# Optimization experiments

Hardware: AMD Instinct MI355X
Metric: run time of the kernel (lower is better)

## Reference

```python
import jax, jax.numpy as jnp
import numpy as np

HIDDEN = 768
NUM_HEADS = 12
HEAD_DIM = HIDDEN // NUM_HEADS
BIAS_SCALE = 0.5


def setup_inputs() -> dict:
    key = jax.random.key(0)
    ks = jax.random.split(key, 8)
    B, S = 4, 2048
    s = 1.0 / np.sqrt(HIDDEN)
    return {
        "hidden_states": jax.random.normal(ks[0], (B, S, HIDDEN), dtype=jnp.float32),
        "attention_mask": jnp.ones((B, S), dtype=jnp.float32),
        "Wq": jax.random.normal(ks[1], (HIDDEN, HIDDEN), dtype=jnp.float32) * s,
        "bq": jnp.zeros((HIDDEN,), dtype=jnp.float32),
        "Wk": jax.random.normal(ks[2], (HIDDEN, HIDDEN), dtype=jnp.float32) * s,
        "bk": jnp.zeros((HIDDEN,), dtype=jnp.float32),
        "Wv": jax.random.normal(ks[3], (HIDDEN, HIDDEN), dtype=jnp.float32) * s,
        "bv": jnp.zeros((HIDDEN,), dtype=jnp.float32),
        "head_bias": jnp.full((NUM_HEADS, 1, 1), 0.1, dtype=jnp.float32),
    }


def _split_heads(x):
    # [B,S,H] -> [B,nh,S,hd]
    B, S, _ = x.shape
    return x.reshape(B, S, NUM_HEADS, HEAD_DIM).transpose(0, 2, 1, 3)


def reference(hidden_states, attention_mask, Wq, bq, Wk, bk, Wv, bv, head_bias):
    q = _split_heads(hidden_states @ Wq.T + bq)
    k = _split_heads(hidden_states @ Wk.T + bk)
    v = _split_heads(hidden_states @ Wv.T + bv)
    # [B,nh,S,S]
    scores = jnp.einsum("bhqd,bhkd->bhqk", q, k) / np.sqrt(HEAD_DIM).astype(np.float32)
    scores = scores + BIAS_SCALE * head_bias  # head_bias broadcasts [nh,1,1]
    ext_mask = (1.0 - attention_mask[:, None, None, :]) * -10000.0
    scores = scores + ext_mask
    probs = jax.nn.softmax(scores, axis=-1)  # dropout is identity in eval
    ctx = jnp.einsum("bhqk,bhkd->bhqd", probs, v)
    B, _, S, _ = ctx.shape
    return ctx.transpose(0, 2, 1, 3).reshape(B, S, HIDDEN)
```

## Files before the change

kernel.cpp:

```cpp
#include <hip/hip_runtime.h>

#define LOG2E 1.44269504088896340736f
#define QSCALE 0.18033688011112042f
#define THR 8.0f

typedef _Float16 half8 __attribute__((ext_vector_type(8)));
typedef _Float16 half4_t __attribute__((ext_vector_type(4)));
typedef __fp16 fp16x2 __attribute__((ext_vector_type(2)));
typedef float f32x4 __attribute__((ext_vector_type(4)));
typedef float f32x16 __attribute__((ext_vector_type(16)));
typedef unsigned int u32x2 __attribute__((ext_vector_type(2)));

__device__ __forceinline__ void gld16(const void* g, void* l) {
  __builtin_amdgcn_global_load_lds(
      (const __attribute__((address_space(1))) void*)g,
      (__attribute__((address_space(3))) void*)l, 16, 0, 0);
}

__global__ void cvt_f32_f16(const float* __restrict__ src, _Float16* __restrict__ dst, int n4) {
  int i = blockIdx.x * blockDim.x + threadIdx.x;
  int st = gridDim.x * blockDim.x;
  for (; i < n4; i += st) {
    float4 v = reinterpret_cast<const float4*>(src)[i];
    half4_t h;
    h[0] = (_Float16)v.x; h[1] = (_Float16)v.y; h[2] = (_Float16)v.z; h[3] = (_Float16)v.w;
    reinterpret_cast<half4_t*>(dst)[i] = h;
  }
}

__global__ void prep_mask(const float* __restrict__ mask, float* __restrict__ mkb, int n) {
  int i = blockIdx.x * blockDim.x + threadIdx.x;
  if (i < n) mkb[i] = (1.0f - mask[i]) * (-10000.0f * LOG2E);
}

__global__ __launch_bounds__(256) void qkv_gemm(
    const _Float16* __restrict__ X,
    const _Float16* __restrict__ Wq, const _Float16* __restrict__ Wk, const _Float16* __restrict__ Wv,
    const float* __restrict__ bq, const float* __restrict__ bk, const float* __restrict__ bv,
    _Float16* __restrict__ qo, _Float16* __restrict__ ko, _Float16* __restrict__ vo) {
  __shared__ _Float16 Al[2][128 * 32];
  __shared__ _Float16 Bl[2][128 * 32];
  const int tid = threadIdx.x;
  const int lane = tid & 63, w = tid >> 6;
  const int wr = w >> 1, wc = w & 1;
  const int mt = blockIdx.x, ntl = blockIdx.y, mode = blockIdx.z;
  const _Float16* W = (mode == 0) ? Wq : (mode == 1) ? Wk : Wv;
  const float* bias = (mode == 0) ? bq : (mode == 1) ? bk : bv;
  _Float16* out = (mode == 0) ? qo : (mode == 1) ? ko : vo;
  const float oscale = (mode == 0) ? QSCALE : 1.0f;

  const _Float16* Xb = X + (size_t)mt * 128 * 768;
  const _Float16* Wb = W + (size_t)ntl * 128 * 768;

  const f32x4 zero4 = {0.f, 0.f, 0.f, 0.f};
  f32x4 acc[4][4];
#pragma unroll
  for (int i = 0; i < 4; ++i)
#pragma unroll
    for (int j = 0; j < 4; ++j) acc[i][j] = zero4;

  auto stage = [&](int bufi, int kt) {
#pragma unroll
    for (int it = 0; it < 2; ++it) {
      int ci = tid + it * 256;
      int row = ci >> 2, c = ci & 3;
      int sw = ((c ^ ((row >> 1) & 3)) << 4);
      gld16((const char*)(Xb + row * 768) + kt * 64 + sw, (char*)&Al[bufi][0] + ci * 16);
      gld16((const char*)(Wb + row * 768) + kt * 64 + sw, (char*)&Bl[bufi][0] + ci * 16);
    }
  };

  stage(0, 0);
  __syncthreads();
  int buf = 0;
  for (int kt = 0; kt < 24; ++kt) {
    if (kt + 1 < 24) stage(buf ^ 1, kt + 1);
    half8 af[4], bf[4];
#pragma unroll
    for (int mi = 0; mi < 4; ++mi) {
      int row = wr * 64 + mi * 16 + (lane & 15);
      int cc = (lane >> 4) ^ ((row >> 1) & 3);
      af[mi] = *(const half8*)((const char*)&Al[buf][0] + row * 64 + cc * 16);
    }
#pragma unroll
    for (int ni = 0; ni < 4; ++ni) {
      int row = wc * 64 + ni * 16 + (lane & 15);
      int cc = (lane >> 4) ^ ((row >> 1) & 3);
      bf[ni] = *(const half8*)((const char*)&Bl[buf][0] + row * 64 + cc * 16);
    }
#pragma unroll
    for (int mi = 0; mi < 4; ++mi)
#pragma unroll
      for (int ni = 0; ni < 4; ++ni)
        acc[mi][ni] = __builtin_amdgcn_mfma_f32_16x16x32_f16(af[mi], bf[ni], acc[mi][ni], 0, 0, 0);
    __syncthreads();
    buf ^= 1;
  }

  const int m0 = mt * 128 + wr * 64, n0 = ntl * 128 + wc * 64;
#pragma unroll
  for (int ni = 0; ni < 4; ++ni) {
    int n = n0 + ni * 16 + (lane & 15);
    float bvv = bias[n];
    int h = n >> 6, d = n & 63;
#pragma unroll
    for (int mi = 0; mi < 4; ++mi) {
      int m = m0 + mi * 16 + ((lane >> 4) << 2);
      int b = m >> 11, s = m & 2047;
      if (mode < 2) {
        _Float16* dst = out + (((size_t)(b * 12 + h) * 2048 + s) * 64 + d);
#pragma unroll
        for (int r = 0; r < 4; ++r) dst[(size_t)r * 64] = (_Float16)((acc[mi][ni][r] + bvv) * oscale);
      } else {
        half4_t pk;
#pragma unroll
        for (int r = 0; r < 4; ++r) pk[r] = (_Float16)(acc[mi][ni][r] + bvv);
        *(half4_t*)(out + ((size_t)(b * 12 + h) * 64 + d) * 2048 + s) = pk;
      }
    }
  }
}

__global__ __launch_bounds__(256) void flash_attn(
    const _Float16* __restrict__ qb, const _Float16* __restrict__ kbuf,
    const _Float16* __restrict__ vtb, const float* __restrict__ mkb,
    float* __restrict__ out) {
  __shared__ _Float16 Kl[2][64 * 64];
  __shared__ _Float16 Vl[2][64 * 64];
  __shared__ float Ml[2048];

  const int tid = threadIdx.x;
  const int lane = tid & 63, w = tid >> 6;
  const int l31 = lane & 31, hi32 = lane >> 5;

  const int i = blockIdx.x;
  const int bh = (i & 7) + 8 * ((i >> 3) >> 4);
  const int qt = (i >> 3) & 15;
  const int b = bh / 12, h = bh % 12;
  const int q0w = qt * 128 + w * 32;

  const _Float16* Kg = kbuf + (size_t)bh * 2048 * 64;
  const _Float16* Vg = vtb + (size_t)bh * 64 * 2048;

  half8 qf[4];
  {
    const _Float16* qp = qb + ((size_t)bh * 2048 + q0w + l31) * 64 + hi32 * 8;
#pragma unroll
    for (int c = 0; c < 4; ++c) qf[c] = *(const half8*)(qp + c * 16);
  }

  auto stage = [&](int nb, int t) {
#pragma unroll
    for (int it = 0; it < 2; ++it) {
      int ci = tid + it * 256;
      int row = ci >> 3, c = ci & 7;
      int sw = ((c ^ (row & 7)) << 4);
      gld16((const char*)Kg + (size_t)t * 8192 + row * 128 + sw, (char*)&Kl[nb][0] + ci * 16);
      gld16((const char*)Vg + (size_t)row * 4096 + t * 128 + sw, (char*)&Vl[nb][0] + ci * 16);
    }
  };

  {
    const char* ms = (const char*)(mkb + (size_t)b * 2048);
#pragma unroll
    for (int it = 0; it < 2; ++it) {
      int ci = tid + it * 256;
      gld16(ms + ci * 16, (char*)Ml + ci * 16);
    }
  }

  f32x16 o[2];
  float m_ = -3.0e4f, l_ = 0.f;
#pragma unroll
  for (int dt = 0; dt < 2; ++dt)
#pragma unroll
    for (int r = 0; r < 16; ++r) o[dt][r] = 0.f;

  stage(0, 0);
  __syncthreads();
  int buf = 0;

  for (int t = 0; t < 32; ++t) {
    if (t + 1 < 32) stage(buf ^ 1, t + 1);

    f32x4 mk[2][4];
    const float* mlt = Ml + t * 64 + hi32 * 4;
#pragma unroll
    for (int kt = 0; kt < 2; ++kt)
#pragma unroll
      for (int g = 0; g < 4; ++g) mk[kt][g] = *(const f32x4*)(mlt + kt * 32 + g * 8);

    const char* kb = (const char*)&Kl[buf][0];
    f32x16 sc[2];
    __builtin_amdgcn_s_setprio(1);
#pragma unroll
    for (int kt = 0; kt < 2; ++kt) {
      int row = kt * 32 + l31;
      const char* krow = kb + row * 128;
      int swz = (row & 7) << 4;
      f32x16 z;
#pragma unroll
      for (int r = 0; r < 16; ++r) z[r] = 0.f;
#pragma unroll
      for (int c = 0; c < 4; ++c) {
        half8 ka = *(const half8*)(krow + ((c * 32 + hi32 * 16) ^ swz));
        z = __builtin_amdgcn_mfma_f32_32x32x16_f16(ka, qf[c], z, 0, 0, 0);
      }
      sc[kt] = z;
    }
    __builtin_amdgcn_s_setprio(0);

#pragma unroll
    for (int kt = 0; kt < 2; ++kt)
#pragma unroll
      for (int r = 0; r < 16; ++r) sc[kt][r] += mk[kt][r >> 2][r & 3];

    float tm[16];
#pragma unroll
    for (int r = 0; r < 16; ++r) tm[r] = fmaxf(sc[0][r], sc[1][r]);
#pragma unroll
    for (int s = 8; s >= 1; s >>= 1)
#pragma unroll
      for (int r = 0; r < s; ++r) tm[r] = fmaxf(tm[r], tm[r + s]);
    float mx;
    {
      union { float f; unsigned u; } a; a.f = tm[0];
      u32x2 sw = __builtin_amdgcn_permlane32_swap(a.u, a.u, false, false);
      union { unsigned u; float f; } plo, phi;
      plo.u = sw[0]; phi.u = sw[1];
      mx = fmaxf(plo.f, phi.f);
    }

    if (!__all(mx <= m_ + THR)) {
      float mn = fmaxf(m_, mx);
      float fcv = __builtin_amdgcn_exp2f(m_ - mn);
      m_ = mn;
      l_ *= fcv;
#pragma unroll
      for (int r = 0; r < 16; ++r) {
        int qrow = (r & 3) + 8 * (r >> 2) + 4 * hi32;
        float fq = __shfl(fcv, qrow);
        o[0][r] *= fq;
        o[1][r] *= fq;
      }
    }

#pragma unroll
    for (int kt = 0; kt < 2; ++kt)
#pragma unroll
      for (int r = 0; r < 16; ++r)
        sc[kt][r] = __builtin_amdgcn_exp2f(sc[kt][r] - m_);

    {
      float ts[16];
#pragma unroll
      for (int r = 0; r < 16; ++r) ts[r] = sc[0][r] + sc[1][r];
#pragma unroll
      for (int s = 8; s >= 1; s >>= 1)
#pragma unroll
        for (int r = 0; r < s; ++r) ts[r] += ts[r + s];
      union { float f; unsigned u; } a; a.f = ts[0];
      u32x2 sw = __builtin_amdgcn_permlane32_swap(a.u, a.u, false, false);
      union { unsigned u; float f; } plo, phi;
      plo.u = sw[0]; phi.u = sw[1];
      l_ += plo.f + phi.f;
    }

    half8 pa[4];
#pragma unroll
    for (int kt = 0; kt < 2; ++kt)
#pragma unroll
      for (int cc = 0; cc < 2; ++cc) {
        int b0 = cc * 8;
        union { fp16x2 h; unsigned u; } u01, u23, u45, u67;
        u01.h = __builtin_amdgcn_cvt_pkrtz(sc[kt][b0 + 0], sc[kt][b0 + 1]);
        u23.h = __builtin_amdgcn_cvt_pkrtz(sc[kt][b0 + 2], sc[kt][b0 + 3]);
        u45.h = __builtin_amdgcn_cvt_pkrtz(sc[kt][b0 + 4], sc[kt][b0 + 5]);
        u67.h = __builtin_amdgcn_cvt_pkrtz(sc[kt][b0 + 6], sc[kt][b0 + 7]);
        u32x2 s1 = __builtin_amdgcn_permlane32_swap(u01.u, u45.u, false, false);
        u32x2 s2 = __builtin_amdgcn_permlane32_swap(u23.u, u67.u, false, false);
        union { unsigned u[4]; half8 hh; } a;
        a.u[0] = s1[0]; a.u[1] = s2[0]; a.u[2] = s1[1]; a.u[3] = s2[1];
        pa[kt * 2 + cc] = a.hh;
      }

    const char* vb = (const char*)&Vl[buf][0];
    __builtin_amdgcn_s_setprio(1);
#pragma unroll
    for (int dt = 0; dt < 2; ++dt) {
      int row = dt * 32 + l31;
      const char* vrow = vb + row * 128;
      int swz = (row & 7) << 4;
#pragma unroll
      for (int ch = 0; ch < 4; ++ch) {
        half8 vbf = *(const half8*)(vrow + ((ch * 32 + hi32 * 16) ^ swz));
        o[dt] = __builtin_amdgcn_mfma_f32_32x32x16_f16(pa[ch], vbf, o[dt], 0, 0, 0);
      }
    }
    __builtin_amdgcn_s_setprio(0);

    __syncthreads();
    buf ^= 1;
  }

  float invl = 1.f / l_;
#pragma unroll
  for (int r = 0; r < 16; ++r) {
    int qrow = (r & 3) + 8 * (r >> 2) + 4 * hi32;
    float iq = __shfl(invl, qrow);
    float* op = out + ((size_t)(b * 2048) + q0w + qrow) * 768 + h * 64 + l31;
    op[0] = o[0][r] * iq;
    op[32] = o[1][r] * iq;
  }
}

extern "C" void kernel_launch(void* const* d_in, const int* in_sizes, int n_in,
                              void* d_out, int out_size, void* d_ws, size_t ws_size,
                              hipStream_t stream) {
  const float* hidden = (const float*)d_in[0];
  const float* mask = (const float*)d_in[1];
  const float* Wq = (const float*)d_in[2];
  const float* bq = (const float*)d_in[3];
  const float* Wk = (const float*)d_in[4];
  const float* bk = (const float*)d_in[5];
  const float* Wv = (const float*)d_in[6];
  const float* bv = (const float*)d_in[7];
  float* out = (float*)d_out;

  char* ws = (char*)d_ws;
  _Float16* hb   = (_Float16*)(ws);
  _Float16* wqb  = (_Float16*)(ws + 12582912);
  _Float16* wkb  = (_Float16*)(ws + 13762560);
  _Float16* wvb  = (_Float16*)(ws + 14942208);
  _Float16* qbuf = (_Float16*)(ws + 16121856);
  _Float16* kbuf = (_Float16*)(ws + 28704768);
  _Float16* vtb  = (_Float16*)(ws + 41287680);
  float* mkb     = (float*)(ws);

  cvt_f32_f16<<<dim3(1024), dim3(256), 0, stream>>>(hidden, hb, 6291456 / 4);
  cvt_f32_f16<<<dim3(288), dim3(256), 0, stream>>>(Wq, wqb, 589824 / 4);
  cvt_f32_f16<<<dim3(288), dim3(256), 0, stream>>>(Wk, wkb, 589824 / 4);
  cvt_f32_f16<<<dim3(288), dim3(256), 0, stream>>>(Wv, wvb, 589824 / 4);

  qkv_gemm<<<dim3(64, 6, 3), dim3(256), 0, stream>>>(hb, wqb, wkb, wvb, bq, bk, bv,
                                                     qbuf, kbuf, vtb);
  prep_mask<<<dim3(32), dim3(256), 0, stream>>>(mask, mkb, 8192);
  flash_attn<<<dim3(768), dim3(256), 0, stream>>>(qbuf, kbuf, vtb, mkb, out);
}
```

Measured before the change: 172.0 us.

## Software-pipeline QK of next tile with softmax-PV of current tile

Restructures the attention main loop into a two-stage software pipeline. K and V are now staged separately, and the QK^T MFMA for tile t+1 is issued alongside softmax and PV for tile t, with ping-pong score registers. Separately, the mask is loaded straight into the MFMA accumulator init, which removes the explicit add. This aims to overlap matrix-core work with the VALU/exp softmax, at the cost of more registers (two score sets) and more complex buffer-index bookkeeping.

Measured after the change: 186.3 us. 1.08x slower.

```diff
diff --git a/kernel.cpp b/kernel.cpp
--- a/kernel.cpp
+++ b/kernel.cpp
@@ -149,25 +149,24 @@
     for (int c = 0; c < 4; ++c) qf[c] = *(const half8*)(qp + c * 16);
   }
 
-  auto stage = [&](int nb, int t) {
+  auto stageK = [&](int nb, int t) {
 #pragma unroll
     for (int it = 0; it < 2; ++it) {
       int ci = tid + it * 256;
       int row = ci >> 3, c = ci & 7;
       int sw = ((c ^ (row & 7)) << 4);
       gld16((const char*)Kg + (size_t)t * 8192 + row * 128 + sw, (char*)&Kl[nb][0] + ci * 16);
-      gld16((const char*)Vg + (size_t)row * 4096 + t * 128 + sw, (char*)&Vl[nb][0] + ci * 16);
-    }
-  };
-
-  {
-    const char* ms = (const char*)(mkb + (size_t)b * 2048);
+    }
+  };
+  auto stageV = [&](int nb, int t) {
 #pragma unroll
     for (int it = 0; it < 2; ++it) {
       int ci = tid + it * 256;
-      gld16(ms + ci * 16, (char*)Ml + ci * 16);
-    }
-  }
+      int row = ci >> 3, c = ci & 7;
+      int sw = ((c ^ (row & 7)) << 4);
+      gld16((const char*)Vg + (size_t)row * 4096 + t * 128 + sw, (char*)&Vl[nb][0] + ci * 16);
+    }
+  };
 
   f32x16 o[2];
   float m_ = -3.0e4f, l_ = 0.f;
@@ -176,31 +175,22 @@
 #pragma unroll
     for (int r = 0; r < 16; ++r) o[dt][r] = 0.f;
 
-  stage(0, 0);
-  __syncthreads();
-  int buf = 0;
-
-  for (int t = 0; t < 32; ++t) {
-    if (t + 1 < 32) stage(buf ^ 1, t + 1);
-
-    f32x4 mk[2][4];
+  auto qk = [&](f32x16* sc, int nb, int t) {
     const float* mlt = Ml + t * 64 + hi32 * 4;
-#pragma unroll
-    for (int kt = 0; kt < 2; ++kt)
-#pragma unroll
-      for (int g = 0; g < 4; ++g) mk[kt][g] = *(const f32x4*)(mlt + kt * 32 + g * 8);
-
-    const char* kb = (const char*)&Kl[buf][0];
-    f32x16 sc[2];
+    const char* kb = (const char*)&Kl[nb][0];
     __builtin_amdgcn_s_setprio(1);
 #pragma unroll
     for (int kt = 0; kt < 2; ++kt) {
+      f32x16 z;
+#pragma unroll
+      for (int g = 0; g < 4; ++g) {
+        f32x4 m4 = *(const f32x4*)(mlt + kt * 32 + g * 8);
+        z[g * 4 + 0] = m4[0]; z[g * 4 + 1] = m4[1];
+        z[g * 4 + 2] = m4[2]; z[g * 4 + 3] = m4[3];
+      }
       int row = kt * 32 + l31;
       const char* krow = kb + row * 128;
       int swz = (row & 7) << 4;
-      f32x16 z;
-#pragma unroll
-      for (int r = 0; r < 16; ++r) z[r] = 0.f;
 #pragma unroll
       for (int c = 0; c < 4; ++c) {
         half8 ka = *(const half8*)(krow + ((c * 32 + hi32 * 16) ^ swz));
@@ -209,12 +199,9 @@
       sc[kt] = z;
     }
     __builtin_amdgcn_s_setprio(0);
-
-#pragma unroll
-    for (int kt = 0; kt < 2; ++kt)
-#pragma unroll
-      for (int r = 0; r < 16; ++r) sc[kt][r] += mk[kt][r >> 2][r & 3];
-
+  };
+
+  auto smpv = [&](f32x16* sc, int nb) {
     float tm[16];
 #pragma unroll
     for (int r = 0; r < 16; ++r) tm[r] = fmaxf(sc[0][r], sc[1][r]);
@@ -272,19 +259,19 @@
 #pragma unroll
       for (int cc = 0; cc < 2; ++cc) {
         int b0 = cc * 8;
-        union { fp16x2 h; unsigned u; } u01, u23, u45, u67;
-        u01.h = __builtin_amdgcn_cvt_pkrtz(sc[kt][b0 + 0], sc[kt][b0 + 1]);
-        u23.h = __builtin_amdgcn_cvt_pkrtz(sc[kt][b0 + 2], sc[kt][b0 + 3]);
-        u45.h = __builtin_amdgcn_cvt_pkrtz(sc[kt][b0 + 4], sc[kt][b0 + 5]);
-        u67.h = __builtin_amdgcn_cvt_pkrtz(sc[kt][b0 + 6], sc[kt][b0 + 7]);
+        union { fp16x2 hh; unsigned u; } u01, u23, u45, u67;
+        u01.hh = __builtin_amdgcn_cvt_pkrtz(sc[kt][b0 + 0], sc[kt][b0 + 1]);
+        u23.hh = __builtin_amdgcn_cvt_pkrtz(sc[kt][b0 + 2], sc[kt][b0 + 3]);
+        u45.hh = __builtin_amdgcn_cvt_pkrtz(sc[kt][b0 + 4], sc[kt][b0 + 5]);
+        u67.hh = __builtin_amdgcn_cvt_pkrtz(sc[kt][b0 + 6], sc[kt][b0 + 7]);
         u32x2 s1 = __builtin_amdgcn_permlane32_swap(u01.u, u45.u, false, false);
         u32x2 s2 = __builtin_amdgcn_permlane32_swap(u23.u, u67.u, false, false);
-        union { unsigned u[4]; half8 hh; } a;
+        union { unsigned u[4]; half8 hv; } a;
         a.u[0] = s1[0]; a.u[1] = s2[0]; a.u[2] = s1[1]; a.u[3] = s2[1];
-        pa[kt * 2 + cc] = a.hh;
-      }
-
-    const char* vb = (const char*)&Vl[buf][0];
+        pa[kt * 2 + cc] = a.hv;
+      }
+
+    const char* vb = (const char*)&Vl[nb][0];
     __builtin_amdgcn_s_setprio(1);
 #pragma unroll
     for (int dt = 0; dt < 2; ++dt) {
@@ -298,9 +285,37 @@
       }
     }
     __builtin_amdgcn_s_setprio(0);
-
+  };
+
+  stageK(0, 0);
+  stageK(1, 1);
+  stageV(0, 0);
+  {
+    const char* ms = (const char*)(mkb + (size_t)b * 2048);
+#pragma unroll
+    for (int it = 0; it < 2; ++it) {
+      int ci = tid + it * 256;
+      gld16(ms + ci * 16, (char*)Ml + ci * 16);
+    }
+  }
+  __syncthreads();
+
+  f32x16 scA[2], scB[2];
+  qk(scA, 0, 0);
+  __syncthreads();
+
+  for (int tt = 0; tt < 32; tt += 2) {
+    if (tt + 2 < 32) stageK(0, tt + 2);
+    stageV(1, tt + 1);
+    qk(scB, 1, tt + 1);
+    smpv(scA, 0);
     __syncthreads();
-    buf ^= 1;
+
+    if (tt + 3 < 32) stageK(1, tt + 3);
+    if (tt + 2 < 32) stageV(0, tt + 2);
+    if (tt + 2 < 32) qk(scA, 0, tt + 2);
+    smpv(scB, 1);
+    __syncthreads();
   }
 
   float invl = 1.f / l_;
```

## Drop LDS staging in flash attention; single-wave blocks read K/V directly from global

Applied to the files above, without the earlier changes.

The attention kernel switches from 256-thread blocks that stage K, V and the mask tile through double-buffered shared memory to 64-thread single-wave blocks (3072 of them) that load K, V and the mask straight from global memory into MFMA operands. The mask is folded in by seeding the MFMA accumulator. This removes the LDS copies and __syncthreads barriers and lets more independent waves run per CU. In exchange, the four waves that share a (batch, head) no longer reuse a single LDS copy of K/V, so global and L2 traffic rises and load latency is no longer overlapped by explicit prefetch.

Measured after the change: 263.9 us. +53.5%, slower.

```diff
diff --git a/kernel.cpp b/kernel.cpp
--- a/kernel.cpp
+++ b/kernel.cpp
@@ -121,26 +121,23 @@
   }
 }
 
-__global__ __launch_bounds__(256) void flash_attn(
+__global__ __launch_bounds__(64, 3) void flash_attn(
     const _Float16* __restrict__ qb, const _Float16* __restrict__ kbuf,
     const _Float16* __restrict__ vtb, const float* __restrict__ mkb,
     float* __restrict__ out) {
-  __shared__ _Float16 Kl[2][64 * 64];
-  __shared__ _Float16 Vl[2][64 * 64];
-  __shared__ float Ml[2048];
-
-  const int tid = threadIdx.x;
-  const int lane = tid & 63, w = tid >> 6;
+  const int lane = threadIdx.x & 63;
   const int l31 = lane & 31, hi32 = lane >> 5;
 
   const int i = blockIdx.x;
-  const int bh = (i & 7) + 8 * ((i >> 3) >> 4);
-  const int qt = (i >> 3) & 15;
+  const int xcd = i & 7, j = i >> 3;
+  const int bh = xcd + 8 * (j >> 6);
+  const int sub = j & 63;
+  const int q0w = (sub >> 2) * 128 + (sub & 3) * 32;
   const int b = bh / 12, h = bh % 12;
-  const int q0w = qt * 128 + w * 32;
 
   const _Float16* Kg = kbuf + (size_t)bh * 2048 * 64;
   const _Float16* Vg = vtb + (size_t)bh * 64 * 2048;
+  const float* mrow = mkb + (size_t)b * 2048 + hi32 * 4;
 
   half8 qf[4];
   {
@@ -149,26 +146,6 @@
     for (int c = 0; c < 4; ++c) qf[c] = *(const half8*)(qp + c * 16);
   }
 
-  auto stage = [&](int nb, int t) {
-#pragma unroll
-    for (int it = 0; it < 2; ++it) {
-      int ci = tid + it * 256;
-      int row = ci >> 3, c = ci & 7;
-      int sw = ((c ^ (row & 7)) << 4);
-      gld16((const char*)Kg + (size_t)t * 8192 + row * 128 + sw, (char*)&Kl[nb][0] + ci * 16);
-      gld16((const char*)Vg + (size_t)row * 4096 + t * 128 + sw, (char*)&Vl[nb][0] + ci * 16);
-    }
-  };
-
-  {
-    const char* ms = (const char*)(mkb + (size_t)b * 2048);
-#pragma unroll
-    for (int it = 0; it < 2; ++it) {
-      int ci = tid + it * 256;
-      gld16(ms + ci * 16, (char*)Ml + ci * 16);
-    }
-  }
-
   f32x16 o[2];
   float m_ = -3.0e4f, l_ = 0.f;
 #pragma unroll
@@ -176,44 +153,28 @@
 #pragma unroll
     for (int r = 0; r < 16; ++r) o[dt][r] = 0.f;
 
-  stage(0, 0);
-  __syncthreads();
-  int buf = 0;
-
   for (int t = 0; t < 32; ++t) {
-    if (t + 1 < 32) stage(buf ^ 1, t + 1);
-
-    f32x4 mk[2][4];
-    const float* mlt = Ml + t * 64 + hi32 * 4;
-#pragma unroll
-    for (int kt = 0; kt < 2; ++kt)
-#pragma unroll
-      for (int g = 0; g < 4; ++g) mk[kt][g] = *(const f32x4*)(mlt + kt * 32 + g * 8);
-
-    const char* kb = (const char*)&Kl[buf][0];
     f32x16 sc[2];
-    __builtin_amdgcn_s_setprio(1);
 #pragma unroll
     for (int kt = 0; kt < 2; ++kt) {
-      int row = kt * 32 + l31;
-      const char* krow = kb + row * 128;
-      int swz = (row & 7) << 4;
       f32x16 z;
-#pragma unroll
-      for (int r = 0; r < 16; ++r) z[r] = 0.f;
+      const float* ml = mrow + t * 64 + kt * 32;
+#pragma unroll
+      for (int g = 0; g < 4; ++g) {
+        f32x4 m4 = *(const f32x4*)(ml + g * 8);
+        z[g * 4 + 0] = m4[0]; z[g * 4 + 1] = m4[1];
+        z[g * 4 + 2] = m4[2]; z[g * 4 + 3] = m4[3];
+      }
+      const _Float16* kr = Kg + (size_t)(t * 64 + kt * 32 + l31) * 64 + hi32 * 8;
+      __builtin_amdgcn_s_setprio(1);
 #pragma unroll
       for (int c = 0; c < 4; ++c) {
-        half8 ka = *(const half8*)(krow + ((c * 32 + hi32 * 16) ^ swz));
+        half8 ka = *(const half8*)(kr + c * 16);
         z = __builtin_amdgcn_mfma_f32_32x32x16_f16(ka, qf[c], z, 0, 0, 0);
       }
+      __builtin_amdgcn_s_setprio(0);
       sc[kt] = z;
     }
-    __builtin_amdgcn_s_setprio(0);
-
-#pragma unroll
-    for (int kt = 0; kt < 2; ++kt)
-#pragma unroll
-      for (int r = 0; r < 16; ++r) sc[kt][r] += mk[kt][r >> 2][r & 3];
 
     float tm[16];
 #pragma unroll
@@ -272,35 +233,29 @@
 #pragma unroll
       for (int cc = 0; cc < 2; ++cc) {
         int b0 = cc * 8;
-        union { fp16x2 h; unsigned u; } u01, u23, u45, u67;
-        u01.h = __builtin_amdgcn_cvt_pkrtz(sc[kt][b0 + 0], sc[kt][b0 + 1]);
-        u23.h = __builtin_amdgcn_cvt_pkrtz(sc[kt][b0 + 2], sc[kt][b0 + 3]);
-        u45.h = __builtin_amdgcn_cvt_pkrtz(sc[kt][b0 + 4], sc[kt][b0 + 5]);
-        u67.h = __builtin_amdgcn_cvt_pkrtz(sc[kt][b0 + 6], sc[kt][b0 + 7]);
+        union { fp16x2 hh; unsigned u; } u01, u23, u45, u67;
+        u01.hh = __builtin_amdgcn_cvt_pkrtz(sc[kt][b0 + 0], sc[kt][b0 + 1]);
+        u23.hh = __builtin_amdgcn_cvt_pkrtz(sc[kt][b0 + 2], sc[kt][b0 + 3]);
+        u45.hh = __builtin_amdgcn_cvt_pkrtz(sc[kt][b0 + 4], sc[kt][b0 + 5]);
+        u67.hh = __builtin_amdgcn_cvt_pkrtz(sc[kt][b0 + 6], sc[kt][b0 + 7]);
         u32x2 s1 = __builtin_amdgcn_permlane32_swap(u01.u, u45.u, false, false);
         u32x2 s2 = __builtin_amdgcn_permlane32_swap(u23.u, u67.u, false, false);
-        union { unsigned u[4]; half8 hh; } a;
+        union { unsigned u[4]; half8 hv; } a;
         a.u[0] = s1[0]; a.u[1] = s2[0]; a.u[2] = s1[1]; a.u[3] = s2[1];
-        pa[kt * 2 + cc] = a.hh;
-      }
-
-    const char* vb = (const char*)&Vl[buf][0];
+        pa[kt * 2 + cc] = a.hv;
+      }
+
     __builtin_amdgcn_s_setprio(1);
 #pragma unroll
     for (int dt = 0; dt < 2; ++dt) {
-      int row = dt * 32 + l31;
-      const char* vrow = vb + row * 128;
-      int swz = (row & 7) << 4;
+      const _Float16* vr = Vg + (size_t)(dt * 32 + l31) * 2048 + t * 64 + hi32 * 8;
 #pragma unroll
       for (int ch = 0; ch < 4; ++ch) {
-        half8 vbf = *(const half8*)(vrow + ((ch * 32 + hi32 * 16) ^ swz));
+        half8 vbf = *(const half8*)(vr + ch * 16);
         o[dt] = __builtin_amdgcn_mfma_f32_32x32x16_f16(pa[ch], vbf, o[dt], 0, 0, 0);
       }
     }
     __builtin_amdgcn_s_setprio(0);
-
-    __syncthreads();
-    buf ^= 1;
   }
 
   float invl = 1.f / l_;
@@ -345,5 +300,5 @@
   qkv_gemm<<<dim3(64, 6, 3), dim3(256), 0, stream>>>(hb, wqb, wkb, wvb, bq, bk, bv,
                                                      qbuf, kbuf, vtb);
   prep_mask<<<dim3(32), dim3(256), 0, stream>>>(mask, mkb, 8192);
-  flash_attn<<<dim3(768), dim3(256), 0, stream>>>(qbuf, kbuf, vtb, mkb, out);
-}
+  flash_attn<<<dim3(3072), dim3(64), 0, stream>>>(qbuf, kbuf, vtb, mkb, out);
+}
```
